# Kernel tuning notes

Measured on AMD Instinct MI355X. Metric: run time of the kernel, lower is better.

Reference implementation:

```python
import jax, jax.numpy as jnp
import numpy as np

INPUT, HIDDEN, Z = 64, 256, 32


def setup_inputs() -> dict:
    key = jax.random.key(0)
    ks = jax.random.split(key, 16)
    B, T = 256, 1024
    s = lambda fan_in: 1.0 / np.sqrt(fan_in)
    u = lambda k, shape, b: jax.random.uniform(k, shape, jnp.float32, -b, b)
    return {
        "x": jax.random.normal(ks[0], (B, T, INPUT), jnp.float32),
        "eps": jax.random.normal(ks[1], (T, B, Z), jnp.float32),
        # encoder q(z|x,h): Linear(hidden+input -> z)
        "enc_mu_W": u(ks[2], (Z, HIDDEN + INPUT), s(HIDDEN + INPUT)),
        "enc_mu_b": u(ks[3], (Z,), s(HIDDEN + INPUT)),
        "enc_sigma_W": u(ks[4], (Z, HIDDEN + INPUT), s(HIDDEN + INPUT)),
        "enc_sigma_b": u(ks[5], (Z,), s(HIDDEN + INPUT)),
        # prior p(z|h): Linear(hidden -> z) (computed but unused, as in source)
        "prior_mu_W": u(ks[6], (Z, HIDDEN), s(HIDDEN)),
        "prior_mu_b": u(ks[7], (Z,), s(HIDDEN)),
        "prior_sigma_W": u(ks[8], (Z, HIDDEN), s(HIDDEN)),
        "prior_sigma_b": u(ks[9], (Z,), s(HIDDEN)),
        # GRU(input+z -> hidden), torch layout: [3H, in], gates order r,z,n
        "W_ih": u(ks[10], (3 * HIDDEN, INPUT + Z), s(HIDDEN)),
        "W_hh": u(ks[11], (3 * HIDDEN, HIDDEN), s(HIDDEN)),
        "b_ih": u(ks[12], (3 * HIDDEN,), s(HIDDEN)),
        "b_hh": u(ks[13], (3 * HIDDEN,), s(HIDDEN)),
    }


def _vrnn(x, eps, enc_mu_W, enc_mu_b, enc_sigma_W, enc_sigma_b,
          prior_mu_W, prior_mu_b, prior_sigma_W, prior_sigma_b,
          W_ih, W_hh, b_ih, b_hh):
    B = x.shape[0]
    x_t_first = jnp.transpose(x, (1, 0, 2))  # [T, B, input]
    h0 = jnp.zeros((B, HIDDEN), x.dtype)

    def step(h, inp):
        x_t, eps_t = inp
        # prior (dead code in source, kept for parity; DCE'd by XLA)
        _p_mu = h @ prior_mu_W.T + prior_mu_b
        _p_lv = h @ prior_sigma_W.T + prior_sigma_b
        enc_in = jnp.concatenate([x_t, h], axis=1)  # [B, input+hidden]
        z_mu = enc_in @ enc_mu_W.T + enc_mu_b
        z_logvar = enc_in @ enc_sigma_W.T + enc_sigma_b
        z_t = z_mu + eps_t * jnp.exp(0.5 * z_logvar)
        gru_in = jnp.concatenate([x_t, z_t], axis=1)  # [B, input+z]
        gi = gru_in @ W_ih.T + b_ih  # [B, 3H]
        gh = h @ W_hh.T + b_hh       # [B, 3H]
        i_r, i_z, i_n = jnp.split(gi, 3, axis=1)
        h_r, h_z, h_n = jnp.split(gh, 3, axis=1)
        r = jax.nn.sigmoid(i_r + h_r)
        u = jax.nn.sigmoid(i_z + h_z)
        n = jnp.tanh(i_n + r * h_n)
        h_new = (1.0 - u) * n + u * h
        return h_new, None

    h_last, _ = jax.lax.scan(step, h0, (x_t_first, eps))
    return h_last  # [B, hidden]


def reference(x, eps, enc_mu_W, enc_mu_b, enc_sigma_W, enc_sigma_b,
              prior_mu_W, prior_mu_b, prior_sigma_W, prior_sigma_b,
              W_ih, W_hh, b_ih, b_hh):
    return _vrnn(x, eps, enc_mu_W, enc_mu_b, enc_sigma_W, enc_sigma_b,
                 prior_mu_W, prior_mu_b, prior_sigma_W, prior_sigma_b,
                 W_ih, W_hh, b_ih, b_hh)
```

## Files before the change

kernel.cpp:

```cpp
#include <hip/hip_runtime.h>
#include <stdint.h>

#define NB 256
#define TSEQ 1024
#define TT_MAX 64

#define REG_P 28
#define LDS_P 48
#define STR_P 52
#define LDSTR 148

typedef _Float16 f16;
typedef _Float16 h2 __attribute__((ext_vector_type(2)));

static __device__ __forceinline__ uint32_t pkh2(float a, float b) {
  h2 v; v[0] = (f16)a; v[1] = (f16)b;
  return __builtin_bit_cast(uint32_t, v);
}

#if __has_builtin(__builtin_amdgcn_fdot2)
static __device__ __forceinline__ float dot2u(uint32_t w, uint32_t h, float c) {
  return __builtin_amdgcn_fdot2(__builtin_bit_cast(h2, w), __builtin_bit_cast(h2, h), c, false);
}
#else
static __device__ __forceinline__ float dot2u(uint32_t w, uint32_t h, float c) {
  h2 a = __builtin_bit_cast(h2, w), b = __builtin_bit_cast(h2, h);
  return c + (float)a[0] * (float)b[0] + (float)a[1] * (float)b[1];
}
#endif

#if __has_builtin(__builtin_amdgcn_rcpf)
#define RCPF(x) __builtin_amdgcn_rcpf(x)
#else
#define RCPF(x) (1.0f / (x))
#endif

static __device__ __forceinline__ float sigm(float x) {
  return RCPF(1.0f + exp2f(-1.44269504f * x));
}
static __device__ __forceinline__ float tanh_f(float x) {
  return 1.0f - 2.0f * RCPF(1.0f + exp2f(2.88539008f * x));
}

__global__ __launch_bounds__(256) void vrnn_pack(
    const float* __restrict__ W_hh, const float* __restrict__ W_ih,
    const float* __restrict__ emW, const float* __restrict__ esW,
    uint32_t* __restrict__ whr, uint32_t* __restrict__ whl,
    uint32_t* __restrict__ whs, uint32_t* __restrict__ whz,
    uint32_t* __restrict__ wep)
{
  const int t = threadIdx.x;
  for (int rr = 0; rr < 3; ++rr) {
    const float* R = W_hh + (size_t)(t + rr * 256) * 256;
    for (int p = 0; p < REG_P; ++p)
      whr[(((size_t)rr * 7 + (p >> 2)) * 256 + t) * 4 + (p & 3)] = pkh2(R[2 * p], R[2 * p + 1]);
    for (int p = 0; p < LDS_P; ++p)
      whl[(size_t)t * LDSTR + rr * LDS_P + p] = pkh2(R[2 * (p + REG_P)], R[2 * (p + REG_P) + 1]);
    for (int p = 0; p < STR_P; ++p)
      whs[(((size_t)rr * 13 + (p >> 2)) * 256 + t) * 4 + (p & 3)] =
          pkh2(R[2 * (p + REG_P + LDS_P)], R[2 * (p + REG_P + LDS_P) + 1]);
    const float* Z = W_ih + (size_t)(t + rr * 256) * 96 + 64;
    for (int p = 0; p < 16; ++p)
      whz[(((size_t)rr * 4 + (p >> 2)) * 256 + t) * 4 + (p & 3)] = pkh2(Z[2 * p], Z[2 * p + 1]);
  }
  const int e = t & 63, s = t >> 6;
  const float* src = (e < 32) ? (emW + (size_t)e * 320 + 64)
                              : (esW + (size_t)(e - 32) * 320 + 64);
  for (int p = 0; p < 32; ++p) {
    int pc = s * 32 + p;
    wep[(((size_t)(p >> 2)) * 256 + t) * 4 + (p & 3)] = pkh2(src[2 * pc], src[2 * pc + 1]);
  }
}

__global__ __launch_bounds__(256, 2) void vrnn_pre(
    const float* __restrict__ x, const float* __restrict__ W_ih,
    const float* __restrict__ b_ih, const float* __restrict__ b_hh,
    const float* __restrict__ emW, const float* __restrict__ emb,
    const float* __restrict__ esW, const float* __restrict__ esb,
    f16* __restrict__ gix, f16* __restrict__ zx,
    int chunk_t0, int TT, int nTT)
{
  const int tid = threadIdx.x;
  const int b  = blockIdx.x / nTT;
  const int tt = blockIdx.x % nTT;
  const int tloc0 = tt * TT;

  uint32_t wx[3][32];
  float bias[3];
  #pragma unroll
  for (int rr = 0; rr < 3; ++rr) {
    int j = tid + rr * 256;
    const float4* wr = (const float4*)(W_ih + (size_t)j * 96);
    #pragma unroll
    for (int p4 = 0; p4 < 16; ++p4) {
      float4 v = wr[p4];
      wx[rr][2 * p4]     = pkh2(v.x, v.y);
      wx[rr][2 * p4 + 1] = pkh2(v.z, v.w);
    }
    bias[rr] = b_ih[j] + (rr < 2 ? b_hh[j] : 0.0f);
  }
  uint32_t we[32]; float ebias = 0.0f;
  if (tid < 64) {
    const float* src = (tid < 32) ? (emW + (size_t)tid * 320)
                                  : (esW + (size_t)(tid - 32) * 320);
    #pragma unroll
    for (int p = 0; p < 32; ++p) we[p] = pkh2(src[2 * p], src[2 * p + 1]);
    ebias = (tid < 32) ? emb[tid] : esb[tid - 32];
  }

  __shared__ uint32_t xs[TT_MAX * 32];
  for (int idx = tid; idx < TT * 32; idx += 256) {
    int tl = idx >> 5, pk = idx & 31;
    size_t base = ((size_t)b * TSEQ + (chunk_t0 + tloc0 + tl)) * 64 + 2 * pk;
    xs[idx] = pkh2(x[base], x[base + 1]);
  }
  __syncthreads();

  for (int tl = 0; tl < TT; ++tl) {
    float a0 = bias[0], a1 = bias[1], a2 = bias[2];
    #pragma unroll
    for (int p = 0; p < 32; ++p) {
      uint32_t u = xs[tl * 32 + p];
      a0 = dot2u(wx[0][p], u, a0);
      a1 = dot2u(wx[1][p], u, a1);
      a2 = dot2u(wx[2][p], u, a2);
    }
    size_t ob = (size_t)(tloc0 + tl) * NB + b;
    f16* g = gix + ob * 768;
    g[tid] = (f16)a0; g[tid + 256] = (f16)a1; g[tid + 512] = (f16)a2;
    if (tid < 64) {
      float a3 = ebias;
      #pragma unroll
      for (int p = 0; p < 32; ++p) a3 = dot2u(we[p], xs[tl * 32 + p], a3);
      zx[ob * 64 + tid] = (f16)a3;
    }
  }
}

__global__ __launch_bounds__(256, 2) void vrnn_rec(
    const f16* __restrict__ gix, const f16* __restrict__ zx,
    const float* __restrict__ eps,
    const uint32_t* __restrict__ whr, const uint32_t* __restrict__ whl_g,
    const uint32_t* __restrict__ whs, const uint32_t* __restrict__ whz,
    const uint32_t* __restrict__ wep_g,
    const float* __restrict__ b_hh,
    float* __restrict__ hws, float* __restrict__ out,
    int t0, int Tlen, int first, int last)
{
  const int t = threadIdx.x;
  const int b = blockIdx.x;

  uint32_t wrg[3][REG_P];
  {
    const uint4* w4 = (const uint4*)whr;
    #pragma unroll
    for (int c = 0; c < 21; ++c) {
      uint4 v = w4[c * 256 + t];
      int rr = c / 7, p4 = c % 7;
      wrg[rr][4 * p4] = v.x; wrg[rr][4 * p4 + 1] = v.y;
      wrg[rr][4 * p4 + 2] = v.z; wrg[rr][4 * p4 + 3] = v.w;
    }
  }
  uint32_t wz[3][16];
  {
    const uint4* w4 = (const uint4*)whz;
    #pragma unroll
    for (int c = 0; c < 12; ++c) {
      uint4 v = w4[c * 256 + t];
      int rr = c / 4, p4 = c % 4;
      wz[rr][4 * p4] = v.x; wz[rr][4 * p4 + 1] = v.y;
      wz[rr][4 * p4 + 2] = v.z; wz[rr][4 * p4 + 3] = v.w;
    }
  }
  uint32_t we[32];
  {
    const uint4* w4 = (const uint4*)wep_g;
    #pragma unroll
    for (int c = 0; c < 8; ++c) {
      uint4 v = w4[c * 256 + t];
      we[4 * c] = v.x; we[4 * c + 1] = v.y; we[4 * c + 2] = v.z; we[4 * c + 3] = v.w;
    }
  }
  #pragma unroll
  for (int rr = 0; rr < 3; ++rr) {
    #pragma unroll
    for (int i = 0; i < REG_P; ++i) asm volatile("" : "+v"(wrg[rr][i]));
    #pragma unroll
    for (int i = 0; i < 16; ++i)   asm volatile("" : "+v"(wz[rr][i]));
  }
  #pragma unroll
  for (int i = 0; i < 32; ++i) asm volatile("" : "+v"(we[i]));
  const float bhn = b_hh[512 + t];

  __shared__ uint32_t lwh[256 * LDSTR];
  __shared__ __align__(16) f16 hf[2][256];
  __shared__ float encp[256];
  __shared__ uint32_t zu[16];

  {
    const uint4* src = (const uint4*)(whl_g + (size_t)t * LDSTR);
    uint4* dst = (uint4*)(lwh + (size_t)t * LDSTR);
    #pragma unroll
    for (int j = 0; j < LDSTR / 4; ++j) dst[j] = src[j];
  }

  float hm = first ? 0.0f : hws[b * 256 + t];
  hf[0][t] = (f16)hm;
  __syncthreads();

  const f16* gp0 = gix + (size_t)b * 768;
  float pf_g0 = (float)gp0[t], pf_g1 = (float)gp0[t + 256], pf_g2 = (float)gp0[t + 512];
  float pf_zm = 0.0f, pf_zl = 0.0f, pf_ep = 0.0f;
  if (t < 32) {
    const f16* zp = zx + (size_t)b * 64;
    pf_zm = (float)zp[t]; pf_zl = (float)zp[32 + t];
    pf_ep = eps[((size_t)t0 * NB + b) * 32 + t];
  }

  const int s = t >> 6;
  const uint32_t* myl = lwh + (size_t)t * LDSTR;
  const uint4* whs4 = (const uint4*)whs;

  uint4 sbuf[13];
  #pragma unroll
  for (int j = 0; j < 13; ++j) sbuf[j] = whs4[j * 256 + t];
  __builtin_amdgcn_sched_barrier(0);

  for (int tl = 0; tl < Tlen; ++tl) {
    const int cur = tl & 1, nxt = cur ^ 1;
    const uint32_t* hu = (const uint32_t*)&hf[cur][0];
    const uint4* hu4 = (const uint4*)hu;

    float ep_ = 0.0f;
    #pragma unroll
    for (int p = 0; p < 32; ++p) {
      ep_ = dot2u(we[p], hu[s * 32 + p], ep_);
    }
    encp[t] = ep_;
    __syncthreads();

    if (t < 32) {
      float mu = pf_zm, lv = pf_zl;
      #pragma unroll
      for (int ss = 0; ss < 4; ++ss) {
        mu += encp[ss * 64 + t];
        lv += encp[ss * 64 + 32 + t];
      }
      float z = mu + pf_ep * exp2f(0.72134752f * lv);
      ((f16*)zu)[t] = (f16)z;
    }
    float g0 = 0.0f, g1 = 0.0f, g2 = 0.0f;
    #pragma unroll
    for (int g4 = 0; g4 < 7; ++g4) {
      uint4 u4 = hu4[g4];
      g0 = dot2u(wrg[0][4 * g4],     u4.x, g0);
      g1 = dot2u(wrg[1][4 * g4],     u4.x, g1);
      g2 = dot2u(wrg[2][4 * g4],     u4.x, g2);
      g0 = dot2u(wrg[0][4 * g4 + 1], u4.y, g0);
      g1 = dot2u(wrg[1][4 * g4 + 1], u4.y, g1);
      g2 = dot2u(wrg[2][4 * g4 + 1], u4.y, g2);
      g0 = dot2u(wrg[0][4 * g4 + 2], u4.z, g0);
      g1 = dot2u(wrg[1][4 * g4 + 2], u4.z, g1);
      g2 = dot2u(wrg[2][4 * g4 + 2], u4.z, g2);
      g0 = dot2u(wrg[0][4 * g4 + 3], u4.w, g0);
      g1 = dot2u(wrg[1][4 * g4 + 3], u4.w, g1);
      g2 = dot2u(wrg[2][4 * g4 + 3], u4.w, g2);
    }
    {
      float a = 0.0f;
      #pragma unroll
      for (int j = 0; j < 13; ++j) {
        uint4 u4 = hu4[19 + j];
        a = dot2u(sbuf[j].x, u4.x, a);
        a = dot2u(sbuf[j].y, u4.y, a);
        a = dot2u(sbuf[j].z, u4.z, a);
        a = dot2u(sbuf[j].w, u4.w, a);
      }
      g0 += a;
    }
    #pragma unroll
    for (int j = 0; j < 13; ++j) sbuf[j] = whs4[(13 + j) * 256 + t];
    __builtin_amdgcn_sched_barrier(0);
    #pragma unroll
    for (int g4 = 0; g4 < 6; ++g4) {
      uint4 u4 = hu4[7 + g4];
      uint4 w0 = *(const uint4*)(myl + 0 * LDS_P + 4 * g4);
      uint4 w1 = *(const uint4*)(myl + 1 * LDS_P + 4 * g4);
      uint4 w2 = *(const uint4*)(myl + 2 * LDS_P + 4 * g4);
      g0 = dot2u(w0.x, u4.x, g0); g1 = dot2u(w1.x, u4.x, g1); g2 = dot2u(w2.x, u4.x, g2);
      g0 = dot2u(w0.y, u4.y, g0); g1 = dot2u(w1.y, u4.y, g1); g2 = dot2u(w2.y, u4.y, g2);
      g0 = dot2u(w0.z, u4.z, g0); g1 = dot2u(w1.z, u4.z, g1); g2 = dot2u(w2.z, u4.z, g2);
      g0 = dot2u(w0.w, u4.w, g0); g1 = dot2u(w1.w, u4.w, g1); g2 = dot2u(w2.w, u4.w, g2);
    }
    {
      float a = 0.0f;
      #pragma unroll
      for (int j = 0; j < 13; ++j) {
        uint4 u4 = hu4[19 + j];
        a = dot2u(sbuf[j].x, u4.x, a);
        a = dot2u(sbuf[j].y, u4.y, a);
        a = dot2u(sbuf[j].z, u4.z, a);
        a = dot2u(sbuf[j].w, u4.w, a);
      }
      g1 += a;
    }
    #pragma unroll
    for (int j = 0; j < 13; ++j) sbuf[j] = whs4[(26 + j) * 256 + t];
    __builtin_amdgcn_sched_barrier(0);
    #pragma unroll
    for (int g4 = 6; g4 < 12; ++g4) {
      uint4 u4 = hu4[7 + g4];
      uint4 w0 = *(const uint4*)(myl + 0 * LDS_P + 4 * g4);
      uint4 w1 = *(const uint4*)(myl + 1 * LDS_P + 4 * g4);
      uint4 w2 = *(const uint4*)(myl + 2 * LDS_P + 4 * g4);
      g0 = dot2u(w0.x, u4.x, g0); g1 = dot2u(w1.x, u4.x, g1); g2 = dot2u(w2.x, u4.x, g2);
      g0 = dot2u(w0.y, u4.y, g0); g1 = dot2u(w1.y, u4.y, g1); g2 = dot2u(w2.y, u4.y, g2);
      g0 = dot2u(w0.z, u4.z, g0); g1 = dot2u(w1.z, u4.z, g1); g2 = dot2u(w2.z, u4.z, g2);
      g0 = dot2u(w0.w, u4.w, g0); g1 = dot2u(w1.w, u4.w, g1); g2 = dot2u(w2.w, u4.w, g2);
    }
    {
      float a = 0.0f;
      #pragma unroll
      for (int j = 0; j < 13; ++j) {
        uint4 u4 = hu4[19 + j];
        a = dot2u(sbuf[j].x, u4.x, a);
        a = dot2u(sbuf[j].y, u4.y, a);
        a = dot2u(sbuf[j].z, u4.z, a);
        a = dot2u(sbuf[j].w, u4.w, a);
      }
      g2 += a;
    }
    __syncthreads();

    float q0 = 0.0f, q1 = 0.0f, q2 = 0.0f;
    #pragma unroll
    for (int p = 0; p < 16; ++p) {
      uint32_t u = zu[p];
      q0 = dot2u(wz[0][p], u, q0);
      q1 = dot2u(wz[1][p], u, q1);
      q2 = dot2u(wz[2][p], u, q2);
    }
    float r  = sigm(pf_g0 + g0 + q0);
    float uu = sigm(pf_g1 + g1 + q1);
    float n  = tanh_f(pf_g2 + q2 + r * (g2 + bhn));
    hm = (1.0f - uu) * n + uu * hm;
    hf[nxt][t] = (f16)hm;

    #pragma unroll
    for (int j = 0; j < 13; ++j) sbuf[j] = whs4[j * 256 + t];
    __builtin_amdgcn_sched_barrier(0);

    int tn = (tl + 1 < Tlen) ? tl + 1 : tl;
    const f16* gp = gix + ((size_t)tn * NB + b) * 768;
    pf_g0 = (float)gp[t]; pf_g1 = (float)gp[t + 256]; pf_g2 = (float)gp[t + 512];
    if (t < 32) {
      const f16* zp = zx + ((size_t)tn * NB + b) * 64;
      pf_zm = (float)zp[t]; pf_zl = (float)zp[32 + t];
      pf_ep = eps[((size_t)(t0 + tn) * NB + b) * 32 + t];
    }
    __syncthreads();
  }

  if (last) out[b * 256 + t] = hm;
  else      hws[b * 256 + t] = hm;
}

extern "C" void kernel_launch(void* const* d_in, const int* in_sizes, int n_in,
                              void* d_out, int out_size, void* d_ws, size_t ws_size,
                              hipStream_t stream) {
  const float* x    = (const float*)d_in[0];
  const float* eps  = (const float*)d_in[1];
  const float* emW  = (const float*)d_in[2];
  const float* emb  = (const float*)d_in[3];
  const float* esW  = (const float*)d_in[4];
  const float* esb  = (const float*)d_in[5];
  const float* W_ih = (const float*)d_in[10];
  const float* W_hh = (const float*)d_in[11];
  const float* b_ih = (const float*)d_in[12];
  const float* b_hh = (const float*)d_in[13];
  float* out = (float*)d_out;

  const size_t o_whr = 262144;
  const size_t o_whl = o_whr + 86016;
  const size_t o_whs = o_whl + 151552;
  const size_t o_whz = o_whs + 159744;
  const size_t o_wep = o_whz + 49152;
  const size_t o_gix = o_wep + 32768;
  int Tc = TSEQ;
  while (Tc > 8 && o_gix + (size_t)Tc * NB * (768 + 64) * 2 > ws_size) Tc >>= 1;

  float*    hws   = (float*)d_ws;
  uint32_t* whr   = (uint32_t*)((char*)d_ws + o_whr);
  uint32_t* whl_g = (uint32_t*)((char*)d_ws + o_whl);
  uint32_t* whs   = (uint32_t*)((char*)d_ws + o_whs);
  uint32_t* whz   = (uint32_t*)((char*)d_ws + o_whz);
  uint32_t* wep   = (uint32_t*)((char*)d_ws + o_wep);
  f16*      gix   = (f16*)((char*)d_ws + o_gix);
  f16*      zx    = gix + (size_t)Tc * NB * 768;

  vrnn_pack<<<dim3(1), dim3(256), 0, stream>>>(W_hh, W_ih, emW, esW,
                                               whr, whl_g, whs, whz, wep);

  int nch = TSEQ / Tc;
  int TT  = Tc < 64 ? Tc : 64;
  int nTT = Tc / TT;

  for (int c = 0; c < nch; ++c) {
    vrnn_pre<<<dim3(NB * nTT), dim3(256), 0, stream>>>(
        x, W_ih, b_ih, b_hh, emW, emb, esW, esb, gix, zx, c * Tc, TT, nTT);
    vrnn_rec<<<dim3(NB), dim3(256), 0, stream>>>(
        gix, zx, eps, whr, whl_g, whs, whz, wep, b_hh, hws, out,
        c * Tc, Tc, c == 0 ? 1 : 0, c == nch - 1 ? 1 : 0);
  }
}
```

Before: 2.975 ms.

## Reduce encoder projection with wave shuffles and drop one barrier per step

The encoder mu/logvar projection is re-partitioned so each group of 4 lanes handles one output row over a quarter of the hidden vector each. The partial sums are combined with xor-shuffles instead of going through an LDS buffer, a barrier and a 32-thread serial reduction. The weight packing is rearranged to match, with a rotation on the h-vector read order to spread LDS bank accesses. Removing the encp buffer and one __syncthreads per timestep shortens the serial critical path of the recurrence, at the cost of extra shuffle instructions.

```diff
diff --git a/kernel.cpp b/kernel.cpp
--- a/kernel.cpp
+++ b/kernel.cpp
@@ -63,12 +63,17 @@
     for (int p = 0; p < 16; ++p)
       whz[(((size_t)rr * 4 + (p >> 2)) * 256 + t) * 4 + (p & 3)] = pkh2(Z[2 * p], Z[2 * p + 1]);
   }
-  const int e = t & 63, s = t >> 6;
-  const float* src = (e < 32) ? (emW + (size_t)e * 320 + 64)
-                              : (esW + (size_t)(e - 32) * 320 + 64);
-  for (int p = 0; p < 32; ++p) {
-    int pc = s * 32 + p;
-    wep[(((size_t)(p >> 2)) * 256 + t) * 4 + (p & 3)] = pkh2(src[2 * pc], src[2 * pc + 1]);
+  {
+    const int l = t & 63, w = t >> 6, rid = l >> 2, kq = l & 3;
+    const int rot2 = (2 * kq) & 7;
+    const int r = (rid < 8) ? (8 * w + rid) : (32 + 8 * w + (rid - 8));
+    const float* esrc = (r < 32) ? (emW + (size_t)r * 320 + 64)
+                                 : (esW + (size_t)(r - 32) * 320 + 64);
+    for (int j = 0; j < 8; ++j)
+      for (int c = 0; c < 4; ++c) {
+        int pc = kq * 32 + ((j + rot2) & 7) * 4 + c;
+        wep[((size_t)j * 256 + t) * 4 + c] = pkh2(esrc[2 * pc], esrc[2 * pc + 1]);
+      }
   }
 }
 
@@ -194,7 +199,6 @@
 
   __shared__ uint32_t lwh[256 * LDSTR];
   __shared__ __align__(16) f16 hf[2][256];
-  __shared__ float encp[256];
   __shared__ uint32_t zu[16];
 
   {
@@ -208,16 +212,20 @@
   hf[0][t] = (f16)hm;
   __syncthreads();
 
+  const int zlane = ((t & 35) == 0);
+  const int ze    = 8 * (t >> 6) + ((t & 31) >> 2);
+  const int base8 = (t & 3) * 8;
+  const int rot2  = (2 * (t & 3)) & 7;
+
   const f16* gp0 = gix + (size_t)b * 768;
   float pf_g0 = (float)gp0[t], pf_g1 = (float)gp0[t + 256], pf_g2 = (float)gp0[t + 512];
   float pf_zm = 0.0f, pf_zl = 0.0f, pf_ep = 0.0f;
-  if (t < 32) {
+  if (zlane) {
     const f16* zp = zx + (size_t)b * 64;
-    pf_zm = (float)zp[t]; pf_zl = (float)zp[32 + t];
-    pf_ep = eps[((size_t)t0 * NB + b) * 32 + t];
-  }
-
-  const int s = t >> 6;
+    pf_zm = (float)zp[ze]; pf_zl = (float)zp[32 + ze];
+    pf_ep = eps[((size_t)t0 * NB + b) * 32 + ze];
+  }
+
   const uint32_t* myl = lwh + (size_t)t * LDSTR;
   const uint4* whs4 = (const uint4*)whs;
 
@@ -231,24 +239,24 @@
     const uint32_t* hu = (const uint32_t*)&hf[cur][0];
     const uint4* hu4 = (const uint4*)hu;
 
-    float ep_ = 0.0f;
-    #pragma unroll
-    for (int p = 0; p < 32; ++p) {
-      ep_ = dot2u(we[p], hu[s * 32 + p], ep_);
-    }
-    encp[t] = ep_;
+    float ep = 0.0f;
+    #pragma unroll
+    for (int j = 0; j < 8; ++j) {
+      uint4 u4 = hu4[base8 + ((j + rot2) & 7)];
+      ep = dot2u(we[4 * j],     u4.x, ep);
+      ep = dot2u(we[4 * j + 1], u4.y, ep);
+      ep = dot2u(we[4 * j + 2], u4.z, ep);
+      ep = dot2u(we[4 * j + 3], u4.w, ep);
+    }
+    ep += __shfl_xor(ep, 1);
+    ep += __shfl_xor(ep, 2);
+    float other = __shfl_xor(ep, 32);
+    if (zlane) {
+      float z = (pf_zm + ep) + pf_ep * exp2f(0.72134752f * (pf_zl + other));
+      ((f16*)zu)[ze] = (f16)z;
+    }
     __syncthreads();
 
-    if (t < 32) {
-      float mu = pf_zm, lv = pf_zl;
-      #pragma unroll
-      for (int ss = 0; ss < 4; ++ss) {
-        mu += encp[ss * 64 + t];
-        lv += encp[ss * 64 + 32 + t];
-      }
-      float z = mu + pf_ep * exp2f(0.72134752f * lv);
-      ((f16*)zu)[t] = (f16)z;
-    }
     float g0 = 0.0f, g1 = 0.0f, g2 = 0.0f;
     #pragma unroll
     for (int g4 = 0; g4 < 7; ++g4) {
@@ -330,7 +338,6 @@
       }
       g2 += a;
     }
-    __syncthreads();
 
     float q0 = 0.0f, q1 = 0.0f, q2 = 0.0f;
     #pragma unroll
@@ -353,10 +360,10 @@
     int tn = (tl + 1 < Tlen) ? tl + 1 : tl;
     const f16* gp = gix + ((size_t)tn * NB + b) * 768;
     pf_g0 = (float)gp[t]; pf_g1 = (float)gp[t + 256]; pf_g2 = (float)gp[t + 512];
-    if (t < 32) {
+    if (zlane) {
       const f16* zp = zx + ((size_t)tn * NB + b) * 64;
-      pf_zm = (float)zp[t]; pf_zl = (float)zp[32 + t];
-      pf_ep = eps[((size_t)(t0 + tn) * NB + b) * 32 + t];
+      pf_zm = (float)zp[ze]; pf_zl = (float)zp[32 + ze];
+      pf_ep = eps[((size_t)(t0 + tn) * NB + b) * 32 + ze];
     }
     __syncthreads();
   }
```

Result: slower. 3.272 ms (+10.0%).

## Split each hidden unit's recurrent dot products across two threads per block

Applied to the files above, without the earlier changes.

The recurrent kernel now uses 512 threads per batch row instead of 256. Each pair of threads splits the 256-wide W_hh row and the z columns in half, and the partial sums are combined with an xor shuffle. The per-thread register, LDS and streamed weight slices are halved and the pack kernel emits the new layout. This shortens each thread's serial dot-product chain per timestep, at the cost of more threads, half of them idle during the gate update, extra shuffles, and a different occupancy profile.

```diff
diff --git a/kernel.cpp b/kernel.cpp
--- a/kernel.cpp
+++ b/kernel.cpp
@@ -5,10 +5,10 @@
 #define TSEQ 1024
 #define TT_MAX 64
 
-#define REG_P 28
-#define LDS_P 48
-#define STR_P 52
-#define LDSTR 148
+#define REG_P 12
+#define LDS_P 24
+#define STR_P 28
+#define LDSTR 76
 
 typedef _Float16 f16;
 typedef _Float16 h2 __attribute__((ext_vector_type(2)));
@@ -42,7 +42,7 @@
   return 1.0f - 2.0f * RCPF(1.0f + exp2f(2.88539008f * x));
 }
 
-__global__ __launch_bounds__(256) void vrnn_pack(
+__global__ __launch_bounds__(512) void vrnn_pack(
     const float* __restrict__ W_hh, const float* __restrict__ W_ih,
     const float* __restrict__ emW, const float* __restrict__ esW,
     uint32_t* __restrict__ whr, uint32_t* __restrict__ whl,
@@ -50,25 +50,37 @@
     uint32_t* __restrict__ wep)
 {
   const int t = threadIdx.x;
+  const int r = t >> 1, q = t & 1;
   for (int rr = 0; rr < 3; ++rr) {
-    const float* R = W_hh + (size_t)(t + rr * 256) * 256;
-    for (int p = 0; p < REG_P; ++p)
-      whr[(((size_t)rr * 7 + (p >> 2)) * 256 + t) * 4 + (p & 3)] = pkh2(R[2 * p], R[2 * p + 1]);
+    const float* R = W_hh + (size_t)(r + rr * 256) * 256 + q * 128;
+    for (int cj = 0; cj < 3; ++cj)
+      for (int i = 0; i < 4; ++i) {
+        int p = cj * 4 + i;
+        whr[(((size_t)rr * 3 + cj) * 512 + t) * 4 + i] = pkh2(R[2 * p], R[2 * p + 1]);
+      }
     for (int p = 0; p < LDS_P; ++p)
       whl[(size_t)t * LDSTR + rr * LDS_P + p] = pkh2(R[2 * (p + REG_P)], R[2 * (p + REG_P) + 1]);
-    for (int p = 0; p < STR_P; ++p)
-      whs[(((size_t)rr * 13 + (p >> 2)) * 256 + t) * 4 + (p & 3)] =
-          pkh2(R[2 * (p + REG_P + LDS_P)], R[2 * (p + REG_P + LDS_P) + 1]);
-    const float* Z = W_ih + (size_t)(t + rr * 256) * 96 + 64;
-    for (int p = 0; p < 16; ++p)
-      whz[(((size_t)rr * 4 + (p >> 2)) * 256 + t) * 4 + (p & 3)] = pkh2(Z[2 * p], Z[2 * p + 1]);
-  }
-  const int e = t & 63, s = t >> 6;
-  const float* src = (e < 32) ? (emW + (size_t)e * 320 + 64)
-                              : (esW + (size_t)(e - 32) * 320 + 64);
-  for (int p = 0; p < 32; ++p) {
-    int pc = s * 32 + p;
-    wep[(((size_t)(p >> 2)) * 256 + t) * 4 + (p & 3)] = pkh2(src[2 * pc], src[2 * pc + 1]);
+    for (int j = 0; j < 7; ++j)
+      for (int i = 0; i < 4; ++i) {
+        int p = 36 + j * 4 + i;
+        whs[(((size_t)rr * 7 + j) * 512 + t) * 4 + i] = pkh2(R[2 * p], R[2 * p + 1]);
+      }
+    const float* Z = W_ih + (size_t)(r + rr * 256) * 96 + 64 + q * 16;
+    for (int cj = 0; cj < 2; ++cj)
+      for (int i = 0; i < 4; ++i) {
+        int p = cj * 4 + i;
+        whz[(((size_t)rr * 2 + cj) * 512 + t) * 4 + i] = pkh2(Z[2 * p], Z[2 * p + 1]);
+      }
+  }
+  {
+    const int e = t & 63, s = t >> 6;
+    const float* esrc = (e < 32) ? (emW + (size_t)e * 320 + 64)
+                                 : (esW + (size_t)(e - 32) * 320 + 64);
+    for (int p4 = 0; p4 < 4; ++p4)
+      for (int i = 0; i < 4; ++i) {
+        int pc = s * 16 + p4 * 4 + i;
+        wep[((size_t)p4 * 512 + t) * 4 + i] = pkh2(esrc[2 * pc], esrc[2 * pc + 1]);
+      }
   }
 }
 
@@ -137,7 +149,7 @@
   }
 }
 
-__global__ __launch_bounds__(256, 2) void vrnn_rec(
+__global__ __launch_bounds__(512) void vrnn_rec(
     const f16* __restrict__ gix, const f16* __restrict__ zx,
     const float* __restrict__ eps,
     const uint32_t* __restrict__ whr, const uint32_t* __restrict__ whl_g,
@@ -149,35 +161,36 @@
 {
   const int t = threadIdx.x;
   const int b = blockIdx.x;
+  const int r = t >> 1, q = t & 1;
 
   uint32_t wrg[3][REG_P];
   {
     const uint4* w4 = (const uint4*)whr;
     #pragma unroll
-    for (int c = 0; c < 21; ++c) {
-      uint4 v = w4[c * 256 + t];
-      int rr = c / 7, p4 = c % 7;
+    for (int c = 0; c < 9; ++c) {
+      uint4 v = w4[c * 512 + t];
+      int rr = c / 3, p4 = c % 3;
       wrg[rr][4 * p4] = v.x; wrg[rr][4 * p4 + 1] = v.y;
       wrg[rr][4 * p4 + 2] = v.z; wrg[rr][4 * p4 + 3] = v.w;
     }
   }
-  uint32_t wz[3][16];
+  uint32_t wz[3][8];
   {
     const uint4* w4 = (const uint4*)whz;
     #pragma unroll
-    for (int c = 0; c < 12; ++c) {
-      uint4 v = w4[c * 256 + t];
-      int rr = c / 4, p4 = c % 4;
+    for (int c = 0; c < 6; ++c) {
+      uint4 v = w4[c * 512 + t];
+      int rr = c / 2, p4 = c % 2;
       wz[rr][4 * p4] = v.x; wz[rr][4 * p4 + 1] = v.y;
       wz[rr][4 * p4 + 2] = v.z; wz[rr][4 * p4 + 3] = v.w;
     }
   }
-  uint32_t we[32];
+  uint32_t we[16];
   {
     const uint4* w4 = (const uint4*)wep_g;
     #pragma unroll
-    for (int c = 0; c < 8; ++c) {
-      uint4 v = w4[c * 256 + t];
+    for (int c = 0; c < 4; ++c) {
+      uint4 v = w4[c * 512 + t];
       we[4 * c] = v.x; we[4 * c + 1] = v.y; we[4 * c + 2] = v.z; we[4 * c + 3] = v.w;
     }
   }
@@ -186,15 +199,15 @@
     #pragma unroll
     for (int i = 0; i < REG_P; ++i) asm volatile("" : "+v"(wrg[rr][i]));
     #pragma unroll
-    for (int i = 0; i < 16; ++i)   asm volatile("" : "+v"(wz[rr][i]));
+    for (int i = 0; i < 8; ++i)    asm volatile("" : "+v"(wz[rr][i]));
   }
   #pragma unroll
-  for (int i = 0; i < 32; ++i) asm volatile("" : "+v"(we[i]));
-  const float bhn = b_hh[512 + t];
-
-  __shared__ uint32_t lwh[256 * LDSTR];
+  for (int i = 0; i < 16; ++i) asm volatile("" : "+v"(we[i]));
+  const float bhn = b_hh[512 + r];
+
+  __shared__ uint32_t lwh[512 * LDSTR];
   __shared__ __align__(16) f16 hf[2][256];
-  __shared__ float encp[256];
+  __shared__ float encp[512];
   __shared__ uint32_t zu[16];
 
   {
@@ -204,12 +217,18 @@
     for (int j = 0; j < LDSTR / 4; ++j) dst[j] = src[j];
   }
 
-  float hm = first ? 0.0f : hws[b * 256 + t];
-  hf[0][t] = (f16)hm;
+  float hm = 0.0f;
+  if (!q) {
+    hm = first ? 0.0f : hws[b * 256 + r];
+    hf[0][r] = (f16)hm;
+  }
   __syncthreads();
 
-  const f16* gp0 = gix + (size_t)b * 768;
-  float pf_g0 = (float)gp0[t], pf_g1 = (float)gp0[t + 256], pf_g2 = (float)gp0[t + 512];
+  float pf_g0 = 0.0f, pf_g1 = 0.0f, pf_g2 = 0.0f;
+  if (!q) {
+    const f16* gp0 = gix + (size_t)b * 768;
+    pf_g0 = (float)gp0[r]; pf_g1 = (float)gp0[r + 256]; pf_g2 = (float)gp0[r + 512];
+  }
   float pf_zm = 0.0f, pf_zl = 0.0f, pf_ep = 0.0f;
   if (t < 32) {
     const f16* zp = zx + (size_t)b * 64;
@@ -218,12 +237,13 @@
   }
 
   const int s = t >> 6;
+  const int bq = q * 16;
   const uint32_t* myl = lwh + (size_t)t * LDSTR;
   const uint4* whs4 = (const uint4*)whs;
 
-  uint4 sbuf[13];
+  uint4 sbuf[7];
   #pragma unroll
-  for (int j = 0; j < 13; ++j) sbuf[j] = whs4[j * 256 + t];
+  for (int j = 0; j < 7; ++j) sbuf[j] = whs4[j * 512 + t];
   __builtin_amdgcn_sched_barrier(0);
 
   for (int tl = 0; tl < Tlen; ++tl) {
@@ -233,8 +253,12 @@
 
     float ep_ = 0.0f;
     #pragma unroll
-    for (int p = 0; p < 32; ++p) {
-      ep_ = dot2u(we[p], hu[s * 32 + p], ep_);
+    for (int p4 = 0; p4 < 4; ++p4) {
+      uint4 u4 = hu4[s * 4 + p4];
+      ep_ = dot2u(we[4 * p4],     u4.x, ep_);
+      ep_ = dot2u(we[4 * p4 + 1], u4.y, ep_);
+      ep_ = dot2u(we[4 * p4 + 2], u4.z, ep_);
+      ep_ = dot2u(we[4 * p4 + 3], u4.w, ep_);
     }
     encp[t] = ep_;
     __syncthreads();
@@ -242,7 +266,7 @@
     if (t < 32) {
       float mu = pf_zm, lv = pf_zl;
       #pragma unroll
-      for (int ss = 0; ss < 4; ++ss) {
+      for (int ss = 0; ss < 8; ++ss) {
         mu += encp[ss * 64 + t];
         lv += encp[ss * 64 + 32 + t];
       }
@@ -251,8 +275,8 @@
     }
     float g0 = 0.0f, g1 = 0.0f, g2 = 0.0f;
     #pragma unroll
-    for (int g4 = 0; g4 < 7; ++g4) {
-      uint4 u4 = hu4[g4];
+    for (int g4 = 0; g4 < 3; ++g4) {
+      uint4 u4 = hu4[bq + g4];
       g0 = dot2u(wrg[0][4 * g4],     u4.x, g0);
       g1 = dot2u(wrg[1][4 * g4],     u4.x, g1);
       g2 = dot2u(wrg[2][4 * g4],     u4.x, g2);
@@ -269,8 +293,8 @@
     {
       float a = 0.0f;
       #pragma unroll
-      for (int j = 0; j < 13; ++j) {
-        uint4 u4 = hu4[19 + j];
+      for (int j = 0; j < 7; ++j) {
+        uint4 u4 = hu4[bq + 9 + j];
         a = dot2u(sbuf[j].x, u4.x, a);
         a = dot2u(sbuf[j].y, u4.y, a);
         a = dot2u(sbuf[j].z, u4.z, a);
@@ -279,11 +303,11 @@
       g0 += a;
     }
     #pragma unroll
-    for (int j = 0; j < 13; ++j) sbuf[j] = whs4[(13 + j) * 256 + t];
+    for (int j = 0; j < 7; ++j) sbuf[j] = whs4[(7 + j) * 512 + t];
     __builtin_amdgcn_sched_barrier(0);
     #pragma unroll
-    for (int g4 = 0; g4 < 6; ++g4) {
-      uint4 u4 = hu4[7 + g4];
+    for (int g4 = 0; g4 < 3; ++g4) {
+      uint4 u4 = hu4[bq + 3 + g4];
       uint4 w0 = *(const uint4*)(myl + 0 * LDS_P + 4 * g4);
       uint4 w1 = *(const uint4*)(myl + 1 * LDS_P + 4 * g4);
       uint4 w2 = *(const uint4*)(myl + 2 * LDS_P + 4 * g4);
@@ -295,8 +319,8 @@
     {
       float a = 0.0f;
       #pragma unroll
-      for (int j = 0; j < 13; ++j) {
-        uint4 u4 = hu4[19 + j];
+      for (int j = 0; j < 7; ++j) {
+        uint4 u4 = hu4[bq + 9 + j];
         a = dot2u(sbuf[j].x, u4.x, a);
         a = dot2u(sbuf[j].y, u4.y, a);
         a = dot2u(sbuf[j].z, u4.z, a);
@@ -305,11 +329,11 @@
       g1 += a;
     }
     #pragma unroll
-    for (int j = 0; j < 13; ++j) sbuf[j] = whs4[(26 + j) * 256 + t];
+    for (int j = 0; j < 7; ++j) sbuf[j] = whs4[(14 + j) * 512 + t];
     __builtin_amdgcn_sched_barrier(0);
     #pragma unroll
-    for (int g4 = 6; g4 < 12; ++g4) {
-      uint4 u4 = hu4[7 + g4];
+    for (int g4 = 3; g4 < 6; ++g4) {
+      uint4 u4 = hu4[bq + 3 + g4];
       uint4 w0 = *(const uint4*)(myl + 0 * LDS_P + 4 * g4);
       uint4 w1 = *(const uint4*)(myl + 1 * LDS_P + 4 * g4);
       uint4 w2 = *(const uint4*)(myl + 2 * LDS_P + 4 * g4);
@@ -321,8 +345,8 @@
     {
       float a = 0.0f;
       #pragma unroll
-      for (int j = 0; j < 13; ++j) {
-        uint4 u4 = hu4[19 + j];
+      for (int j = 0; j < 7; ++j) {
+        uint4 u4 = hu4[bq + 9 + j];
         a = dot2u(sbuf[j].x, u4.x, a);
         a = dot2u(sbuf[j].y, u4.y, a);
         a = dot2u(sbuf[j].z, u4.z, a);
@@ -334,25 +358,31 @@
 
     float q0 = 0.0f, q1 = 0.0f, q2 = 0.0f;
     #pragma unroll
-    for (int p = 0; p < 16; ++p) {
-      uint32_t u = zu[p];
+    for (int p = 0; p < 8; ++p) {
+      uint32_t u = zu[q * 8 + p];
       q0 = dot2u(wz[0][p], u, q0);
       q1 = dot2u(wz[1][p], u, q1);
       q2 = dot2u(wz[2][p], u, q2);
     }
-    float r  = sigm(pf_g0 + g0 + q0);
-    float uu = sigm(pf_g1 + g1 + q1);
-    float n  = tanh_f(pf_g2 + q2 + r * (g2 + bhn));
-    hm = (1.0f - uu) * n + uu * hm;
-    hf[nxt][t] = (f16)hm;
-
-    #pragma unroll
-    for (int j = 0; j < 13; ++j) sbuf[j] = whs4[j * 256 + t];
+    g0 += __shfl_xor(g0, 1); g1 += __shfl_xor(g1, 1); g2 += __shfl_xor(g2, 1);
+    q0 += __shfl_xor(q0, 1); q1 += __shfl_xor(q1, 1); q2 += __shfl_xor(q2, 1);
+    if (!q) {
+      float rg = sigm(pf_g0 + g0 + q0);
+      float uu = sigm(pf_g1 + g1 + q1);
+      float n  = tanh_f(pf_g2 + q2 + rg * (g2 + bhn));
+      hm = (1.0f - uu) * n + uu * hm;
+      hf[nxt][r] = (f16)hm;
+    }
+
+    #pragma unroll
+    for (int j = 0; j < 7; ++j) sbuf[j] = whs4[j * 512 + t];
     __builtin_amdgcn_sched_barrier(0);
 
     int tn = (tl + 1 < Tlen) ? tl + 1 : tl;
-    const f16* gp = gix + ((size_t)tn * NB + b) * 768;
-    pf_g0 = (float)gp[t]; pf_g1 = (float)gp[t + 256]; pf_g2 = (float)gp[t + 512];
+    if (!q) {
+      const f16* gp = gix + ((size_t)tn * NB + b) * 768;
+      pf_g0 = (float)gp[r]; pf_g1 = (float)gp[r + 256]; pf_g2 = (float)gp[r + 512];
+    }
     if (t < 32) {
       const f16* zp = zx + ((size_t)tn * NB + b) * 64;
       pf_zm = (float)zp[t]; pf_zl = (float)zp[32 + t];
@@ -361,8 +391,10 @@
     __syncthreads();
   }
 
-  if (last) out[b * 256 + t] = hm;
-  else      hws[b * 256 + t] = hm;
+  if (!q) {
+    if (last) out[b * 256 + r] = hm;
+    else      hws[b * 256 + r] = hm;
+  }
 }
 
 extern "C" void kernel_launch(void* const* d_in, const int* in_sizes, int n_in,
@@ -381,9 +413,9 @@
   float* out = (float*)d_out;
 
   const size_t o_whr = 262144;
-  const size_t o_whl = o_whr + 86016;
-  const size_t o_whs = o_whl + 151552;
-  const size_t o_whz = o_whs + 159744;
+  const size_t o_whl = o_whr + 73728;
+  const size_t o_whs = o_whl + 155648;
+  const size_t o_whz = o_whs + 172032;
   const size_t o_wep = o_whz + 49152;
   const size_t o_gix = o_wep + 32768;
   int Tc = TSEQ;
@@ -398,7 +430,7 @@
   f16*      gix   = (f16*)((char*)d_ws + o_gix);
   f16*      zx    = gix + (size_t)Tc * NB * 768;
 
-  vrnn_pack<<<dim3(1), dim3(256), 0, stream>>>(W_hh, W_ih, emW, esW,
+  vrnn_pack<<<dim3(1), dim3(512), 0, stream>>>(W_hh, W_ih, emW, esW,
                                                whr, whl_g, whs, whz, wep);
 
   int nch = TSEQ / Tc;
@@ -408,7 +440,7 @@
   for (int c = 0; c < nch; ++c) {
     vrnn_pre<<<dim3(NB * nTT), dim3(256), 0, stream>>>(
         x, W_ih, b_ih, b_hh, emW, emb, esW, esb, gix, zx, c * Tc, TT, nTT);
-    vrnn_rec<<<dim3(NB), dim3(256), 0, stream>>>(
+    vrnn_rec<<<dim3(NB), dim3(512), 0, stream>>>(
         gix, zx, eps, whr, whl_g, whs, whz, wep, b_hh, hws, out,
         c * Tc, Tc, c == 0 ? 1 : 0, c == nch - 1 ? 1 : 0);
   }
```

Result: faster. 2.822 ms (-5.1%).
